# Performance work log

Hardware: AMD Instinct MI355X
Metric: run time of the kernel (lower is better)

The kernel has to match this reference:

```python
import jax, jax.numpy as jnp
import numpy as np

B = 262144
INPUT_DIM = 4
NUM_STEPS = 50          # int(0.5 / 0.01)
H = 0.01                # time_step
SIGMA, RHO, BETA = 10.0, 28.0, 8.0 / 3.0
COUPLING_STRENGTH = 1.0


def _xavier(key, fan_in, fan_out):
    limit = float(np.sqrt(6.0 / (fan_in + fan_out)))
    return jax.random.uniform(key, (fan_in, fan_out), jnp.float32, -limit, limit)


def setup_inputs() -> dict:
    key = jax.random.key(0)
    ks = jax.random.split(key, 7)
    features = jax.random.normal(ks[0], (B, INPUT_DIM), jnp.float32)
    return {
        "features": features,
        # initial_state_mapper: Linear(4,16) -> tanh -> Linear(16,3) -> tanh
        "W1": _xavier(ks[1], INPUT_DIM, 16), "b1": jnp.zeros((16,), jnp.float32),
        "W2": _xavier(ks[2], 16, 3),         "b2": jnp.zeros((3,), jnp.float32),
        # coupling_mapper: Linear(4,8) -> tanh -> Linear(8,3) -> tanh
        "Wc1": _xavier(ks[3], INPUT_DIM, 8), "bc1": jnp.zeros((8,), jnp.float32),
        "Wc2": _xavier(ks[4], 8, 3),         "bc2": jnp.zeros((3,), jnp.float32),
        # param_adapter: Linear(4,8) -> relu -> Linear(8,3) -> sigmoid
        "Wp1": _xavier(ks[5], INPUT_DIM, 8), "bp1": jnp.zeros((8,), jnp.float32),
        "Wp2": _xavier(ks[6], 8, 3),         "bp2": jnp.zeros((3,), jnp.float32),
    }


def _lorenz(state, coupling, params):
    x, y, z = state[:, 0], state[:, 1], state[:, 2]
    s, r, b = params[:, 0], params[:, 1], params[:, 2]
    dx = s * (y - x) + coupling[:, 0]
    dy = x * (r - z) - y + coupling[:, 1]
    dz = x * y - b * z + coupling[:, 2]
    return jnp.stack([dx, dy, dz], axis=1)


def _rk4(state, coupling, params):
    k1 = _lorenz(state, coupling, params)
    k2 = _lorenz(state + 0.5 * H * k1, coupling, params)
    k3 = _lorenz(state + 0.5 * H * k2, coupling, params)
    k4 = _lorenz(state + H * k3, coupling, params)
    return state + (H / 6.0) * (k1 + 2.0 * k2 + 2.0 * k3 + k4)


def reference(features, W1, b1, W2, b2, Wc1, bc1, Wc2, bc2, Wp1, bp1, Wp2, bp2):
    # initial states, scaled by 2
    init = jnp.tanh(jnp.tanh(features @ W1 + b1) @ W2 + b2) * 2.0
    # couplings
    coup = jnp.tanh(jnp.tanh(features @ Wc1 + bc1) @ Wc2 + bc2) * COUPLING_STRENGTH
    # adapted lorenz parameters
    scales = jax.nn.sigmoid(jax.nn.relu(features @ Wp1 + bp1) @ Wp2 + bp2)
    params = jnp.stack([
        SIGMA * (0.5 + scales[:, 0]),
        RHO * (0.5 + scales[:, 1]),
        BETA * (0.5 + scales[:, 2]),
    ], axis=1)

    def step(state, _):
        nxt = _rk4(state, coup, params)
        return nxt, nxt

    _, traj = jax.lax.scan(step, init, None, length=NUM_STEPS - 1)  # [T-1, B, 3]
    traj = jnp.concatenate([init[None], traj], axis=0)              # [T, B, 3]
    return jnp.transpose(traj, (1, 0, 2))                           # [B, T, 3]
```

## Files before the change

### kernel.cpp

```cpp
#include <hip/hip_runtime.h>

#define NSTEP 50
#define RND 2
#define ROWW 75
#define NT 64

__device__ __forceinline__ void lorenz(float x, float y, float z,
                                       float S, float R, float Bb,
                                       float c0, float c1, float c2,
                                       float& dx, float& dy, float& dz) {
    dx = S * (y - x) + c0;
    dy = x * (R - z) - y + c1;
    dz = x * y - Bb * z + c2;
}

__device__ __forceinline__ unsigned int bpack(float lo, float hi) {
    unsigned int a = (__builtin_bit_cast(unsigned int, lo) + 0x8000u) >> 16;
    unsigned int b = (__builtin_bit_cast(unsigned int, hi) + 0x8000u) & 0xFFFF0000u;
    return a | b;
}
__device__ __forceinline__ float bunpack_lo(unsigned int w) {
    return __builtin_bit_cast(float, w << 16);
}
__device__ __forceinline__ float bunpack_hi(unsigned int w) {
    return __builtin_bit_cast(float, w & 0xFFFF0000u);
}

__device__ __forceinline__ float tanh_fast(float x) {
    float e = __expf(2.0f * x);
    float r = __builtin_amdgcn_rcpf(e + 1.0f);
    return __builtin_fmaf(-2.0f, r, 1.0f);
}
__device__ __forceinline__ float sigmoid_fast(float x) {
    float e = __expf(-x);
    return __builtin_amdgcn_rcpf(1.0f + e);
}

__device__ __forceinline__ void lds_fence() {
    asm volatile("s_waitcnt lgkmcnt(0)" ::: "memory");
}

__global__ __launch_bounds__(NT, 2) void chaotic_embed_kernel(
    const float* __restrict__ features,
    const float* __restrict__ W1,  const float* __restrict__ b1,
    const float* __restrict__ W2,  const float* __restrict__ b2,
    const float* __restrict__ Wc1, const float* __restrict__ bc1,
    const float* __restrict__ Wc2, const float* __restrict__ bc2,
    const float* __restrict__ Wp1, const float* __restrict__ bp1,
    const float* __restrict__ Wp2, const float* __restrict__ bp2,
    float* __restrict__ out)
{
    __shared__ unsigned int tile[NT * ROWW];
    const int lane = threadIdx.x;
    const long pbase = (long)blockIdx.x * (NT * RND);

    const float4 f40 = ((const float4*)features)[pbase + lane];
    const float4 f41 = ((const float4*)features)[pbase + NT + lane];

    unsigned int* row = tile + lane * ROWW;

    for (int r = 0; r < RND; ++r) {
        const float4 f4 = r ? f41 : f40;
        const float fv[4] = {f4.x, f4.y, f4.z, f4.w};

        float h1[16];
        #pragma unroll
        for (int j = 0; j < 16; ++j) {
            float a = b1[j];
            #pragma unroll
            for (int i = 0; i < 4; ++i) a = __builtin_fmaf(fv[i], W1[i * 16 + j], a);
            h1[j] = tanh_fast(a);
        }
        float init[3];
        #pragma unroll
        for (int c = 0; c < 3; ++c) {
            float a = b2[c];
            #pragma unroll
            for (int j = 0; j < 16; ++j) a = __builtin_fmaf(h1[j], W2[j * 3 + c], a);
            init[c] = 2.0f * tanh_fast(a);
        }
        float hc[8];
        #pragma unroll
        for (int j = 0; j < 8; ++j) {
            float a = bc1[j];
            #pragma unroll
            for (int i = 0; i < 4; ++i) a = __builtin_fmaf(fv[i], Wc1[i * 8 + j], a);
            hc[j] = tanh_fast(a);
        }
        float coup[3];
        #pragma unroll
        for (int c = 0; c < 3; ++c) {
            float a = bc2[c];
            #pragma unroll
            for (int j = 0; j < 8; ++j) a = __builtin_fmaf(hc[j], Wc2[j * 3 + c], a);
            coup[c] = tanh_fast(a);
        }
        float hp[8];
        #pragma unroll
        for (int j = 0; j < 8; ++j) {
            float a = bp1[j];
            #pragma unroll
            for (int i = 0; i < 4; ++i) a = __builtin_fmaf(fv[i], Wp1[i * 8 + j], a);
            hp[j] = fmaxf(a, 0.0f);
        }
        float sc[3];
        #pragma unroll
        for (int c = 0; c < 3; ++c) {
            float a = bp2[c];
            #pragma unroll
            for (int j = 0; j < 8; ++j) a = __builtin_fmaf(hp[j], Wp2[j * 3 + c], a);
            sc[c] = sigmoid_fast(a);
        }
        const float S  = 10.0f * (0.5f + sc[0]);
        const float R  = 28.0f * (0.5f + sc[1]);
        const float Bb = (8.0f / 3.0f) * (0.5f + sc[2]);
        const float c0 = coup[0], c1 = coup[1], c2 = coup[2];
        const float H = 0.01f, HH = 0.5f * 0.01f, H6 = 0.01f / 6.0f;

        float sx = init[0], sy = init[1], sz = init[2];
        float px, py, pz;

        auto step = [&]() {
            float k1x, k1y, k1z, k2x, k2y, k2z, k3x, k3y, k3z, k4x, k4y, k4z;
            lorenz(sx, sy, sz, S, R, Bb, c0, c1, c2, k1x, k1y, k1z);
            lorenz(sx + HH * k1x, sy + HH * k1y, sz + HH * k1z,
                   S, R, Bb, c0, c1, c2, k2x, k2y, k2z);
            lorenz(sx + HH * k2x, sy + HH * k2y, sz + HH * k2z,
                   S, R, Bb, c0, c1, c2, k3x, k3y, k3z);
            lorenz(sx + H * k3x, sy + H * k3y, sz + H * k3z,
                   S, R, Bb, c0, c1, c2, k4x, k4y, k4z);
            sx += H6 * (k1x + 2.0f * k2x + 2.0f * k3x + k4x);
            sy += H6 * (k1y + 2.0f * k2y + 2.0f * k3y + k4y);
            sz += H6 * (k1z + 2.0f * k2z + 2.0f * k3z + k4z);
        };

        {
            px = sx; py = sy; pz = sz;
            step();
            row[0] = bpack(px, py);
            row[1] = bpack(pz, sx);
            row[2] = bpack(sy, sz);
        }
        #pragma unroll 2
        for (int g = 1; g < 25; ++g) {
            step();
            px = sx; py = sy; pz = sz;
            step();
            row[3 * g + 0] = bpack(px, py);
            row[3 * g + 1] = bpack(pz, sx);
            row[3 * g + 2] = bpack(sy, sz);
        }

        lds_fence();

        float4* __restrict__ outv =
            (float4*)out + (long)blockIdx.x * (RND * 2400) + r * 2400;
        const uint2* __restrict__ img2 = (const uint2*)tile;
        #pragma unroll 4
        for (int k = 0; k < 38; ++k) {
            const int i = 64 * k + lane;
            if (k < 37 || lane < 32) {
                const uint2 ww = img2[i];
                float4 v;
                v.x = bunpack_lo(ww.x);
                v.y = bunpack_hi(ww.x);
                v.z = bunpack_lo(ww.y);
                v.w = bunpack_hi(ww.y);
                outv[i] = v;
            }
        }

        lds_fence();
    }
}

extern "C" void kernel_launch(void* const* d_in, const int* in_sizes, int n_in,
                              void* d_out, int out_size, void* d_ws, size_t ws_size,
                              hipStream_t stream) {
    const float* features = (const float*)d_in[0];
    const float* W1  = (const float*)d_in[1];
    const float* b1  = (const float*)d_in[2];
    const float* W2  = (const float*)d_in[3];
    const float* b2  = (const float*)d_in[4];
    const float* Wc1 = (const float*)d_in[5];
    const float* bc1 = (const float*)d_in[6];
    const float* Wc2 = (const float*)d_in[7];
    const float* bc2 = (const float*)d_in[8];
    const float* Wp1 = (const float*)d_in[9];
    const float* bp1 = (const float*)d_in[10];
    const float* Wp2 = (const float*)d_in[11];
    const float* bp2 = (const float*)d_in[12];
    float* out = (float*)d_out;

    const int B = in_sizes[0] / 4;
    const int grid = B / (NT * RND);

    chaotic_embed_kernel<<<grid, NT, 0, stream>>>(
        features, W1, b1, W2, b2, Wc1, bc1, Wc2, bc2,
        Wp1, bp1, Wp2, bp2, out);
}
```

Before: 51.63 us.

## Overlap first-half trajectory stores with second-half RK4 integration per sample

Each block now handles one 64-sample round instead of two, with a smaller LDS region and launch bounds raised to 4 blocks per CU. The first 24 timesteps are staged in LDS. Their global writes are interleaved with the computation of the remaining timesteps, which are held in registers and then flushed through LDS. The goal is to hide store latency behind RK4 arithmetic and raise occupancy. In exchange, the stores become 8-byte float2 writes with division-based indexing instead of float4, which adds register pressure and integer arithmetic.

```diff
diff --git a/kernel.cpp b/kernel.cpp
--- a/kernel.cpp
+++ b/kernel.cpp
@@ -1,9 +1,10 @@
 #include <hip/hip_runtime.h>
 
+#define NT 64
 #define NSTEP 50
-#define RND 2
-#define ROWW 75
-#define NT 64
+#define AW 36
+#define BW 39
+#define RSTR 39
 
 __device__ __forceinline__ void lorenz(float x, float y, float z,
                                        float S, float R, float Bb,
@@ -40,7 +41,7 @@
     asm volatile("s_waitcnt lgkmcnt(0)" ::: "memory");
 }
 
-__global__ __launch_bounds__(NT, 2) void chaotic_embed_kernel(
+__global__ __launch_bounds__(NT, 4) void chaotic_embed_kernel(
     const float* __restrict__ features,
     const float* __restrict__ W1,  const float* __restrict__ b1,
     const float* __restrict__ W2,  const float* __restrict__ b2,
@@ -50,127 +51,147 @@
     const float* __restrict__ Wp2, const float* __restrict__ bp2,
     float* __restrict__ out)
 {
-    __shared__ unsigned int tile[NT * ROWW];
+    __shared__ unsigned int region[NT * RSTR];
+
     const int lane = threadIdx.x;
-    const long pbase = (long)blockIdx.x * (NT * RND);
-
-    const float4 f40 = ((const float4*)features)[pbase + lane];
-    const float4 f41 = ((const float4*)features)[pbase + NT + lane];
-
-    unsigned int* row = tile + lane * ROWW;
-
-    for (int r = 0; r < RND; ++r) {
-        const float4 f4 = r ? f41 : f40;
-        const float fv[4] = {f4.x, f4.y, f4.z, f4.w};
-
-        float h1[16];
-        #pragma unroll
-        for (int j = 0; j < 16; ++j) {
-            float a = b1[j];
-            #pragma unroll
-            for (int i = 0; i < 4; ++i) a = __builtin_fmaf(fv[i], W1[i * 16 + j], a);
-            h1[j] = tanh_fast(a);
+    const long pbase = (long)blockIdx.x * NT;
+
+    const float4 f4 = ((const float4*)features)[pbase + lane];
+    const float fv[4] = {f4.x, f4.y, f4.z, f4.w};
+
+    float h1[16];
+    #pragma unroll
+    for (int j = 0; j < 16; ++j) {
+        float a = b1[j];
+        #pragma unroll
+        for (int i = 0; i < 4; ++i) a = __builtin_fmaf(fv[i], W1[i * 16 + j], a);
+        h1[j] = tanh_fast(a);
+    }
+    float init[3];
+    #pragma unroll
+    for (int c = 0; c < 3; ++c) {
+        float a = b2[c];
+        #pragma unroll
+        for (int j = 0; j < 16; ++j) a = __builtin_fmaf(h1[j], W2[j * 3 + c], a);
+        init[c] = 2.0f * tanh_fast(a);
+    }
+    float hc[8];
+    #pragma unroll
+    for (int j = 0; j < 8; ++j) {
+        float a = bc1[j];
+        #pragma unroll
+        for (int i = 0; i < 4; ++i) a = __builtin_fmaf(fv[i], Wc1[i * 8 + j], a);
+        hc[j] = tanh_fast(a);
+    }
+    float coup[3];
+    #pragma unroll
+    for (int c = 0; c < 3; ++c) {
+        float a = bc2[c];
+        #pragma unroll
+        for (int j = 0; j < 8; ++j) a = __builtin_fmaf(hc[j], Wc2[j * 3 + c], a);
+        coup[c] = tanh_fast(a);
+    }
+    float hp[8];
+    #pragma unroll
+    for (int j = 0; j < 8; ++j) {
+        float a = bp1[j];
+        #pragma unroll
+        for (int i = 0; i < 4; ++i) a = __builtin_fmaf(fv[i], Wp1[i * 8 + j], a);
+        hp[j] = fmaxf(a, 0.0f);
+    }
+    float sc[3];
+    #pragma unroll
+    for (int c = 0; c < 3; ++c) {
+        float a = bp2[c];
+        #pragma unroll
+        for (int j = 0; j < 8; ++j) a = __builtin_fmaf(hp[j], Wp2[j * 3 + c], a);
+        sc[c] = sigmoid_fast(a);
+    }
+    const float S  = 10.0f * (0.5f + sc[0]);
+    const float R  = 28.0f * (0.5f + sc[1]);
+    const float Bb = (8.0f / 3.0f) * (0.5f + sc[2]);
+    const float c0 = coup[0], c1 = coup[1], c2 = coup[2];
+    const float H = 0.01f, HH = 0.5f * 0.01f, H6 = 0.01f / 6.0f;
+
+    float sx = init[0], sy = init[1], sz = init[2];
+    float px, py, pz;
+
+    auto step = [&]() {
+        float k1x, k1y, k1z, k2x, k2y, k2z, k3x, k3y, k3z, k4x, k4y, k4z;
+        lorenz(sx, sy, sz, S, R, Bb, c0, c1, c2, k1x, k1y, k1z);
+        lorenz(sx + HH * k1x, sy + HH * k1y, sz + HH * k1z,
+               S, R, Bb, c0, c1, c2, k2x, k2y, k2z);
+        lorenz(sx + HH * k2x, sy + HH * k2y, sz + HH * k2z,
+               S, R, Bb, c0, c1, c2, k3x, k3y, k3z);
+        lorenz(sx + H * k3x, sy + H * k3y, sz + H * k3z,
+               S, R, Bb, c0, c1, c2, k4x, k4y, k4z);
+        sx += H6 * (k1x + 2.0f * k2x + 2.0f * k3x + k4x);
+        sy += H6 * (k1y + 2.0f * k2y + 2.0f * k3y + k4y);
+        sz += H6 * (k1z + 2.0f * k2z + 2.0f * k3z + k4z);
+    };
+
+    unsigned int* row = region + lane * RSTR;
+
+    {
+        px = sx; py = sy; pz = sz;
+        step();
+        row[0] = bpack(px, py);
+        row[1] = bpack(pz, sx);
+        row[2] = bpack(sy, sz);
+    }
+    #pragma unroll
+    for (int g = 1; g < 12; ++g) {
+        step();
+        px = sx; py = sy; pz = sz;
+        step();
+        row[3 * g + 0] = bpack(px, py);
+        row[3 * g + 1] = bpack(pz, sx);
+        row[3 * g + 2] = bpack(sy, sz);
+    }
+
+    lds_fence();
+
+    float* __restrict__ outW = out + pbase * 150;
+
+    unsigned int rb[39];
+    constexpr int fend[14] = {0,3,6,9,11,14,17,20,22,25,28,31,33,36};
+    #pragma unroll
+    for (int g = 0; g < 13; ++g) {
+        step();
+        px = sx; py = sy; pz = sz;
+        step();
+        rb[3 * g + 0] = bpack(px, py);
+        rb[3 * g + 1] = bpack(pz, sx);
+        rb[3 * g + 2] = bpack(sy, sz);
+        #pragma unroll
+        for (int k = fend[g]; k < fend[g + 1]; ++k) {
+            const int i  = 64 * k + lane;
+            const int pp = i / 36;
+            const int sl = i - 36 * pp;
+            const unsigned int v = region[pp * RSTR + sl];
+            float2 o;
+            o.x = bunpack_lo(v);
+            o.y = bunpack_hi(v);
+            *(float2*)(outW + pp * 150 + 2 * sl) = o;
         }
-        float init[3];
-        #pragma unroll
-        for (int c = 0; c < 3; ++c) {
-            float a = b2[c];
-            #pragma unroll
-            for (int j = 0; j < 16; ++j) a = __builtin_fmaf(h1[j], W2[j * 3 + c], a);
-            init[c] = 2.0f * tanh_fast(a);
-        }
-        float hc[8];
-        #pragma unroll
-        for (int j = 0; j < 8; ++j) {
-            float a = bc1[j];
-            #pragma unroll
-            for (int i = 0; i < 4; ++i) a = __builtin_fmaf(fv[i], Wc1[i * 8 + j], a);
-            hc[j] = tanh_fast(a);
-        }
-        float coup[3];
-        #pragma unroll
-        for (int c = 0; c < 3; ++c) {
-            float a = bc2[c];
-            #pragma unroll
-            for (int j = 0; j < 8; ++j) a = __builtin_fmaf(hc[j], Wc2[j * 3 + c], a);
-            coup[c] = tanh_fast(a);
-        }
-        float hp[8];
-        #pragma unroll
-        for (int j = 0; j < 8; ++j) {
-            float a = bp1[j];
-            #pragma unroll
-            for (int i = 0; i < 4; ++i) a = __builtin_fmaf(fv[i], Wp1[i * 8 + j], a);
-            hp[j] = fmaxf(a, 0.0f);
-        }
-        float sc[3];
-        #pragma unroll
-        for (int c = 0; c < 3; ++c) {
-            float a = bp2[c];
-            #pragma unroll
-            for (int j = 0; j < 8; ++j) a = __builtin_fmaf(hp[j], Wp2[j * 3 + c], a);
-            sc[c] = sigmoid_fast(a);
-        }
-        const float S  = 10.0f * (0.5f + sc[0]);
-        const float R  = 28.0f * (0.5f + sc[1]);
-        const float Bb = (8.0f / 3.0f) * (0.5f + sc[2]);
-        const float c0 = coup[0], c1 = coup[1], c2 = coup[2];
-        const float H = 0.01f, HH = 0.5f * 0.01f, H6 = 0.01f / 6.0f;
-
-        float sx = init[0], sy = init[1], sz = init[2];
-        float px, py, pz;
-
-        auto step = [&]() {
-            float k1x, k1y, k1z, k2x, k2y, k2z, k3x, k3y, k3z, k4x, k4y, k4z;
-            lorenz(sx, sy, sz, S, R, Bb, c0, c1, c2, k1x, k1y, k1z);
-            lorenz(sx + HH * k1x, sy + HH * k1y, sz + HH * k1z,
-                   S, R, Bb, c0, c1, c2, k2x, k2y, k2z);
-            lorenz(sx + HH * k2x, sy + HH * k2y, sz + HH * k2z,
-                   S, R, Bb, c0, c1, c2, k3x, k3y, k3z);
-            lorenz(sx + H * k3x, sy + H * k3y, sz + H * k3z,
-                   S, R, Bb, c0, c1, c2, k4x, k4y, k4z);
-            sx += H6 * (k1x + 2.0f * k2x + 2.0f * k3x + k4x);
-            sy += H6 * (k1y + 2.0f * k2y + 2.0f * k3y + k4y);
-            sz += H6 * (k1z + 2.0f * k2z + 2.0f * k3z + k4z);
-        };
-
-        {
-            px = sx; py = sy; pz = sz;
-            step();
-            row[0] = bpack(px, py);
-            row[1] = bpack(pz, sx);
-            row[2] = bpack(sy, sz);
-        }
-        #pragma unroll 2
-        for (int g = 1; g < 25; ++g) {
-            step();
-            px = sx; py = sy; pz = sz;
-            step();
-            row[3 * g + 0] = bpack(px, py);
-            row[3 * g + 1] = bpack(pz, sx);
-            row[3 * g + 2] = bpack(sy, sz);
-        }
-
-        lds_fence();
-
-        float4* __restrict__ outv =
-            (float4*)out + (long)blockIdx.x * (RND * 2400) + r * 2400;
-        const uint2* __restrict__ img2 = (const uint2*)tile;
-        #pragma unroll 4
-        for (int k = 0; k < 38; ++k) {
-            const int i = 64 * k + lane;
-            if (k < 37 || lane < 32) {
-                const uint2 ww = img2[i];
-                float4 v;
-                v.x = bunpack_lo(ww.x);
-                v.y = bunpack_hi(ww.x);
-                v.z = bunpack_lo(ww.y);
-                v.w = bunpack_hi(ww.y);
-                outv[i] = v;
-            }
-        }
-
-        lds_fence();
+    }
+
+    lds_fence();
+
+    #pragma unroll
+    for (int s = 0; s < 39; ++s) row[s] = rb[s];
+    lds_fence();
+
+    #pragma unroll 4
+    for (int k = 0; k < 39; ++k) {
+        const int i  = 64 * k + lane;
+        const int pp = i / 39;
+        const int sl = i - 39 * pp;
+        const unsigned int v = region[i];
+        float2 o;
+        o.x = bunpack_lo(v);
+        o.y = bunpack_hi(v);
+        *(float2*)(outW + pp * 150 + 72 + 2 * sl) = o;
     }
 }
 
@@ -193,7 +214,7 @@
     float* out = (float*)d_out;
 
     const int B = in_sizes[0] / 4;
-    const int grid = B / (NT * RND);
+    const int grid = B / NT;
 
     chaotic_embed_kernel<<<grid, NT, 0, stream>>>(
         features, W1, b1, W2, b2, Wc1, bc1, Wc2, bc2,
```

Result: slower. 54.89 us (+6.3%).
